# Performance work log

Measured on AMD Instinct MI355X. Metric: run time of the kernel, lower is better.

## Reference

```python
import jax, jax.numpy as jnp
import numpy as np

HIDDEN = 256
N_HEADS = 8
HEAD_DIM = HIDDEN // N_HEADS
SCALE = HEAD_DIM ** -0.5
LN_EPS = 1e-5


def entmax15(z):
    """Entmax-1.5 along the last axis (Peters et al. 2019 exact algorithm)."""
    z = z / 2.0
    z = z - jnp.max(z, axis=-1, keepdims=True)
    zs = jnp.flip(jnp.sort(z, axis=-1), axis=-1)          # descending
    K = z.shape[-1]
    k = jnp.arange(1, K + 1, dtype=z.dtype)
    mean = jnp.cumsum(zs, axis=-1) / k
    mean_sq = jnp.cumsum(zs * zs, axis=-1) / k
    ss = k * (mean_sq - mean * mean)
    delta = (1.0 - ss) / k
    tau = mean - jnp.sqrt(jnp.maximum(delta, 1e-12))
    support = (tau <= zs).astype(jnp.int32)
    k_star = jnp.sum(support, axis=-1, keepdims=True)      # support size >=1
    tau_star = jnp.take_along_axis(tau, k_star - 1, axis=-1)
    p = jnp.square(jnp.maximum(z - tau_star, 0.0))
    return p


def _attend(q, kv, W_q, W_k, W_v, log_temp):
    B, K, H = kv.shape
    qh = (q @ W_q.T).reshape(B, N_HEADS, HEAD_DIM)                 # (B,n,d)
    kh = (kv @ W_k.T).reshape(B, K, N_HEADS, HEAD_DIM)             # (B,K,n,d)
    vh = (kv @ W_v.T).reshape(B, K, N_HEADS, HEAD_DIM)
    scores = jnp.einsum('bnd,bknd->bnk', qh, kh) * (SCALE * jnp.exp(log_temp))
    attn = entmax15(scores)                                        # (B,n,K) sparse
    ctx = jnp.einsum('bnk,bknd->bnd', attn, vh).reshape(B, H)
    return ctx


def layernorm(x, gamma, beta):
    mu = jnp.mean(x, axis=-1, keepdims=True)
    var = jnp.mean(jnp.square(x - mu), axis=-1, keepdims=True)
    return (x - mu) * jax.lax.rsqrt(var + LN_EPS) * gamma + beta


def setup_inputs() -> dict:
    key = jax.random.key(0)
    ks = jax.random.split(key, 12)
    B, K, H = 32, 8192, HIDDEN
    s = 0.02
    return {
        'z_gene': jax.random.normal(ks[0], (B, H), jnp.float32),
        'z_cpg_seq': jax.random.normal(ks[1], (B, K, H), jnp.float32),
        'z_mirna_seq': jax.random.normal(ks[2], (B, K, H), jnp.float32),
        'W_q': jax.random.normal(ks[3], (H, H), jnp.float32) * s,
        'W_k_cpg': jax.random.normal(ks[4], (H, H), jnp.float32) * s,
        'W_v_cpg': jax.random.normal(ks[5], (H, H), jnp.float32) * s,
        'W_k_mirna': jax.random.normal(ks[6], (H, H), jnp.float32) * s,
        'W_v_mirna': jax.random.normal(ks[7], (H, H), jnp.float32) * s,
        'W_out': jax.random.normal(ks[8], (H, 2 * H), jnp.float32) * s,
        'b_out': jnp.zeros((H,), jnp.float32),
        'ln_gamma': jnp.ones((H,), jnp.float32),
        'ln_beta': jnp.zeros((H,), jnp.float32),
        'modality_logits': jnp.zeros((2,), jnp.float32),
        'log_temp': jnp.zeros((), jnp.float32),
    }


def reference(z_gene, z_cpg_seq, z_mirna_seq, W_q, W_k_cpg, W_v_cpg,
              W_k_mirna, W_v_mirna, W_out, b_out, ln_gamma, ln_beta,
              modality_logits, log_temp):
    ctx_cpg = _attend(z_gene, z_cpg_seq, W_q, W_k_cpg, W_v_cpg, log_temp)
    ctx_mirna = _attend(z_gene, z_mirna_seq, W_q, W_k_mirna, W_v_mirna, log_temp)
    w = jax.nn.softmax(modality_logits)
    combined = jnp.concatenate([w[0] * ctx_cpg, w[1] * ctx_mirna], axis=-1)
    fused = layernorm(combined @ W_out.T + b_out + z_gene, ln_gamma, ln_beta)
    return fused
```

## Files before the change

kernel.cpp:

```cpp
#include <hip/hip_runtime.h>
#include <cstdint>
#include <cstddef>

#define HIDDEN 256
#define NHEADS 8
#define HDIM 32
#define KLEN 8192
#define BATCH 32
#define NCHUNK 16
#define CHUNK (KLEN / NCHUNK)
#define LN_EPS 1e-5f

#define OFF_QT   ((size_t)0)
#define SZ_QT    ((size_t)2*BATCH*NHEADS*HIDDEN)
#define OFF_SC   (OFF_QT + SZ_QT)
#define SZ_SC    ((size_t)2*BATCH*KLEN*NHEADS)
#define OFF_TAU  (OFF_SC + SZ_SC)
#define SZ_TAU   ((size_t)2*BATCH*NHEADS)
#define OFF_UP   (OFF_TAU + SZ_TAU)
#define SZ_UP    ((size_t)2*BATCH*NCHUNK*NHEADS*HIDDEN)
#define OFF_COMB (OFF_UP + SZ_UP)
#define SZ_COMB  ((size_t)BATCH*2*HIDDEN)

__global__ void k_prep(const float* __restrict__ zg, const float* __restrict__ Wq,
                       const float* __restrict__ Wk0, const float* __restrict__ Wk1,
                       const float* __restrict__ log_temp, float* __restrict__ qt) {
    int b = blockIdx.x, t = threadIdx.x;
    __shared__ float z[HIDDEN];
    __shared__ float qh[HIDDEN];
    z[t] = zg[(size_t)b*HIDDEN + t];
    __syncthreads();
    const float4* wr4 = (const float4*)(Wq + (size_t)t*HIDDEN);
    const float4* z4 = (const float4*)z;
    float acc = 0.f;
    #pragma unroll 8
    for (int i = 0; i < HIDDEN/4; ++i) {
        float4 w = wr4[i], zz = z4[i];
        acc += w.x*zz.x + w.y*zz.y + w.z*zz.z + w.w*zz.w;
    }
    qh[t] = acc;
    __syncthreads();
    float alpha = 0.5f * rsqrtf((float)HDIM) * __expf(log_temp[0]);
    for (int m = 0; m < 2; ++m) {
        const float* Wk = m ? Wk1 : Wk0;
        for (int n = 0; n < NHEADS; ++n) {
            float a = 0.f;
            #pragma unroll 8
            for (int d = 0; d < HDIM; ++d) {
                a += qh[n*HDIM + d] * Wk[(size_t)(n*HDIM + d)*HIDDEN + t];
            }
            qt[(((size_t)m*BATCH + b)*NHEADS + n)*HIDDEN + t] = a * alpha;
        }
    }
}

__global__ void __launch_bounds__(256) k_scores(const float* __restrict__ kv0,
                                                const float* __restrict__ kv1,
                                                const float* __restrict__ qt,
                                                float* __restrict__ sc) {
    int bid = blockIdx.x;
    int chunk = bid % NCHUNK;
    int m = (bid / NCHUNK) & 1;
    int b = bid / (2*NCHUNK);
    int t = threadIdx.x;
    int wave = t >> 6;
    int g    = (t >> 3) & 7;
    int seg  = t & 7;
    __shared__ float lq[NHEADS*260];
    const float* qtg = qt + ((size_t)m*BATCH + b)*NHEADS*HIDDEN;
    #pragma unroll
    for (int i = 0; i < 8; ++i) {
        int j = t + i*256;
        lq[(j >> 8)*260 + (j & 255)] = qtg[j];
    }
    __syncthreads();
    const float* kv = (m ? kv1 : kv0) + (size_t)b*KLEN*HIDDEN;
    const float4* kv4 = (const float4*)kv;
    float* out = sc + ((size_t)m*BATCH + b)*KLEN*NHEADS;
    int b0 = seg & 1, b1 = (seg >> 1) & 1, b2 = (seg >> 2) & 1;

    int rowbase = chunk*CHUNK + wave*128;
    for (int pass = 0; pass < 8; ++pass) {
        size_t r0 = (size_t)rowbase + pass*16 + g*2;
        size_t r1 = r0 + 1;
        float4 kva[8], kvb[8];
        #pragma unroll
        for (int i = 0; i < 8; ++i) kva[i] = kv4[r0*64 + i*8 + seg];
        #pragma unroll
        for (int i = 0; i < 8; ++i) kvb[i] = kv4[r1*64 + i*8 + seg];
        float acc0[8], acc1[8];
        #pragma unroll
        for (int n = 0; n < 8; ++n) { acc0[n] = 0.f; acc1[n] = 0.f; }
        #pragma unroll
        for (int n = 0; n < 8; ++n) {
            const float4* qn4 = (const float4*)(lq + n*260);
            #pragma unroll
            for (int i = 0; i < 8; ++i) {
                float4 q = qn4[i*8 + seg];
                acc0[n] += kva[i].x*q.x + kva[i].y*q.y + kva[i].z*q.z + kva[i].w*q.w;
                acc1[n] += kvb[i].x*q.x + kvb[i].y*q.y + kvb[i].z*q.z + kvb[i].w*q.w;
            }
        }
        float w0[4], w1[4];
        #pragma unroll
        for (int j = 0; j < 4; ++j) {
            float k0 = b0 ? acc0[2*j+1] : acc0[2*j];
            float s0 = b0 ? acc0[2*j]   : acc0[2*j+1];
            w0[j] = k0 + __shfl_xor(s0, 1);
            float k1 = b0 ? acc1[2*j+1] : acc1[2*j];
            float s1 = b0 ? acc1[2*j]   : acc1[2*j+1];
            w1[j] = k1 + __shfl_xor(s1, 1);
        }
        float x0[2], x1[2];
        #pragma unroll
        for (int j = 0; j < 2; ++j) {
            float k0 = b1 ? w0[2*j+1] : w0[2*j];
            float s0 = b1 ? w0[2*j]   : w0[2*j+1];
            x0[j] = k0 + __shfl_xor(s0, 2);
            float k1 = b1 ? w1[2*j+1] : w1[2*j];
            float s1 = b1 ? w1[2*j]   : w1[2*j+1];
            x1[j] = k1 + __shfl_xor(s1, 2);
        }
        float ka = b2 ? x0[1] : x0[0];
        float sa = b2 ? x0[0] : x0[1];
        float y0 = ka + __shfl_xor(sa, 4);
        float kb = b2 ? x1[1] : x1[0];
        float sb = b2 ? x1[0] : x1[1];
        float y1 = kb + __shfl_xor(sb, 4);
        out[r0*8 + seg] = y0;
        out[r1*8 + seg] = y1;
    }
}

__global__ void __launch_bounds__(256) k_entmax(const float* __restrict__ sc,
                                                float* __restrict__ tau) {
    int bid = blockIdx.x;
    int n = bid & 7, b = (bid >> 3) & 31, m = bid >> 8;
    int t = threadIdx.x;
    __shared__ float zs[KLEN];
    __shared__ float red[4];
    const float* src = sc + ((size_t)m*BATCH + b)*KLEN*NHEADS + n;
    float mx = -1e30f;
    #pragma unroll
    for (int i = 0; i < KLEN/256; ++i) {
        float v = src[(size_t)(t + i*256)*NHEADS];
        zs[t + i*256] = v;
        mx = fmaxf(mx, v);
    }
    for (int off = 32; off; off >>= 1) mx = fmaxf(mx, __shfl_xor(mx, off));
    if ((t & 63) == 0) red[t >> 6] = mx;
    __syncthreads();
    mx = fmaxf(fmaxf(red[0], red[1]), fmaxf(red[2], red[3]));
    __syncthreads();
    const float4* z4 = (const float4*)zs;
    float lo = mx - 1.0f, hi = mx;
    for (int it = 0; it < 30; ++it) {
        float tm = 0.5f*(lo + hi);
        float s = 0.f;
        #pragma unroll
        for (int i = 0; i < 8; ++i) {
            float4 zz = z4[t + i*256];
            float d;
            d = fmaxf(zz.x - tm, 0.f); s = fmaf(d, d, s);
            d = fmaxf(zz.y - tm, 0.f); s = fmaf(d, d, s);
            d = fmaxf(zz.z - tm, 0.f); s = fmaf(d, d, s);
            d = fmaxf(zz.w - tm, 0.f); s = fmaf(d, d, s);
        }
        for (int off = 32; off; off >>= 1) s += __shfl_xor(s, off);
        if ((t & 63) == 0) red[t >> 6] = s;
        __syncthreads();
        s = red[0] + red[1] + red[2] + red[3];
        __syncthreads();
        if (s >= 1.0f) lo = tm; else hi = tm;
    }
    if (t == 0) tau[bid] = 0.5f*(lo + hi);
}

__global__ void __launch_bounds__(256) k_ctxsum(const float* __restrict__ kv0,
                                                const float* __restrict__ kv1,
                                                const float* __restrict__ sc,
                                                const float* __restrict__ tau,
                                                float* __restrict__ upart) {
    int bid = blockIdx.x;
    int chunk = bid % NCHUNK;
    int m = (bid / NCHUNK) & 1;
    int b = bid / (2*NCHUNK);
    int t = threadIdx.x;
    int wave = t >> 6, lane = t & 63;
    const float* kv = (m ? kv1 : kv0) + (size_t)b*KLEN*HIDDEN;
    const float4* kv4 = (const float4*)kv;
    const float* zrow = sc + ((size_t)m*BATCH + b)*KLEN*NHEADS;
    const float4* zrow4 = (const float4*)zrow;
    float tv[8];
    #pragma unroll
    for (int n = 0; n < 8; ++n) tv[n] = tau[((size_t)m*BATCH + b)*NHEADS + n];
    float acc[8][4];
    #pragma unroll
    for (int n = 0; n < 8; ++n)
        #pragma unroll
        for (int c = 0; c < 4; ++c) acc[n][c] = 0.f;

    #pragma unroll 2
    for (int kk = wave; kk < CHUNK; kk += 4) {
        size_t k = (size_t)chunk*CHUNK + kk;
        float4 kvv = kv4[k*64 + lane];
        float4 za = zrow4[k*2], zb = zrow4[k*2 + 1];
        float p[8], d;
        d = fmaxf(za.x - tv[0], 0.f); p[0] = d*d;
        d = fmaxf(za.y - tv[1], 0.f); p[1] = d*d;
        d = fmaxf(za.z - tv[2], 0.f); p[2] = d*d;
        d = fmaxf(za.w - tv[3], 0.f); p[3] = d*d;
        d = fmaxf(zb.x - tv[4], 0.f); p[4] = d*d;
        d = fmaxf(zb.y - tv[5], 0.f); p[5] = d*d;
        d = fmaxf(zb.z - tv[6], 0.f); p[6] = d*d;
        d = fmaxf(zb.w - tv[7], 0.f); p[7] = d*d;
        #pragma unroll
        for (int n = 0; n < 8; ++n) {
            acc[n][0] = fmaf(p[n], kvv.x, acc[n][0]);
            acc[n][1] = fmaf(p[n], kvv.y, acc[n][1]);
            acc[n][2] = fmaf(p[n], kvv.z, acc[n][2]);
            acc[n][3] = fmaf(p[n], kvv.w, acc[n][3]);
        }
    }
    __shared__ float redls[4*NHEADS*HIDDEN];
    float4* red4 = (float4*)redls;
    #pragma unroll
    for (int n = 0; n < 8; ++n) {
        float4 v; v.x = acc[n][0]; v.y = acc[n][1]; v.z = acc[n][2]; v.w = acc[n][3];
        red4[((size_t)wave*8 + n)*64 + lane] = v;
    }
    __syncthreads();
    float* up = upart + (((size_t)m*BATCH + b)*NCHUNK + chunk)*NHEADS*HIDDEN;
    int n = t >> 5, hq = (t & 31)*2;
    #pragma unroll
    for (int j = 0; j < 2; ++j) {
        float4 s = red4[((size_t)0*8 + n)*64 + hq + j];
        #pragma unroll
        for (int w = 1; w < 4; ++w) {
            float4 v = red4[((size_t)w*8 + n)*64 + hq + j];
            s.x += v.x; s.y += v.y; s.z += v.z; s.w += v.w;
        }
        ((float4*)(up + (size_t)n*HIDDEN))[hq + j] = s;
    }
}

__global__ void k_ctx(const float* __restrict__ upart, const float* __restrict__ Wv0,
                      const float* __restrict__ Wv1, const float* __restrict__ mlogits,
                      float* __restrict__ comb) {
    int b = blockIdx.x, t = threadIdx.x;
    __shared__ float ul[NHEADS*260];
    float l0 = mlogits[0], l1 = mlogits[1];
    float mxl = fmaxf(l0, l1);
    float e0 = __expf(l0 - mxl), e1 = __expf(l1 - mxl);
    float w0 = e0/(e0 + e1), w1 = e1/(e0 + e1);
    for (int m = 0; m < 2; ++m) {
        const float* Wv = m ? Wv1 : Wv0;
        float wm = m ? w1 : w0;
        __syncthreads();
        for (int n = 0; n < NHEADS; ++n) {
            float s = 0.f;
            const float* up = upart + ((size_t)m*BATCH + b)*NCHUNK*NHEADS*HIDDEN
                              + (size_t)n*HIDDEN + t;
            #pragma unroll
            for (int c = 0; c < NCHUNK; ++c) s += up[(size_t)c*NHEADS*HIDDEN];
            ul[n*260 + t] = s;
        }
        __syncthreads();
        int n = t >> 5;
        const float4* wr4 = (const float4*)(Wv + (size_t)t*HIDDEN);
        const float4* uu4 = (const float4*)(ul + n*260);
        float acc = 0.f;
        #pragma unroll 8
        for (int i = 0; i < HIDDEN/4; ++i) {
            float4 w = wr4[i], uu = uu4[i];
            acc += w.x*uu.x + w.y*uu.y + w.z*uu.z + w.w*uu.w;
        }
        comb[(size_t)b*(2*HIDDEN) + (size_t)m*HIDDEN + t] = acc * wm;
    }
}

__global__ void k_out(const float* __restrict__ comb, const float* __restrict__ Wout,
                      const float* __restrict__ bout, const float* __restrict__ zg,
                      const float* __restrict__ gamma, const float* __restrict__ beta,
                      float* __restrict__ out) {
    int b = blockIdx.x, t = threadIdx.x;
    __shared__ float cl[2*HIDDEN];
    __shared__ float red[4];
    cl[t] = comb[(size_t)b*512 + t];
    cl[t + 256] = comb[(size_t)b*512 + 256 + t];
    __syncthreads();
    float acc = bout[t] + zg[(size_t)b*HIDDEN + t];
    const float4* wr4 = (const float4*)(Wout + (size_t)t*512);
    const float4* cl4 = (const float4*)cl;
    #pragma unroll 8
    for (int i = 0; i < 512/4; ++i) {
        float4 w = wr4[i], c = cl4[i];
        acc += w.x*c.x + w.y*c.y + w.z*c.z + w.w*c.w;
    }
    float s = acc;
    for (int off = 32; off; off >>= 1) s += __shfl_xor(s, off);
    if ((t & 63) == 0) red[t >> 6] = s;
    __syncthreads();
    float mu = (red[0] + red[1] + red[2] + red[3]) * (1.0f/HIDDEN);
    __syncthreads();
    float dv = acc - mu;
    float vs = dv*dv;
    for (int off = 32; off; off >>= 1) vs += __shfl_xor(vs, off);
    if ((t & 63) == 0) red[t >> 6] = vs;
    __syncthreads();
    float var = (red[0] + red[1] + red[2] + red[3]) * (1.0f/HIDDEN);
    out[(size_t)b*HIDDEN + t] = dv * rsqrtf(var + LN_EPS) * gamma[t] + beta[t];
}

extern "C" void kernel_launch(void* const* d_in, const int* in_sizes, int n_in,
                              void* d_out, int out_size, void* d_ws, size_t ws_size,
                              hipStream_t stream) {
    const float* zg    = (const float*)d_in[0];
    const float* cpg   = (const float*)d_in[1];
    const float* mir   = (const float*)d_in[2];
    const float* Wq    = (const float*)d_in[3];
    const float* Wk0   = (const float*)d_in[4];
    const float* Wv0   = (const float*)d_in[5];
    const float* Wk1   = (const float*)d_in[6];
    const float* Wv1   = (const float*)d_in[7];
    const float* Wout  = (const float*)d_in[8];
    const float* bout  = (const float*)d_in[9];
    const float* gam   = (const float*)d_in[10];
    const float* bet   = (const float*)d_in[11];
    const float* mlog  = (const float*)d_in[12];
    const float* ltemp = (const float*)d_in[13];

    float* ws   = (float*)d_ws;
    float* qt   = ws + OFF_QT;
    float* sc   = ws + OFF_SC;
    float* tau  = ws + OFF_TAU;
    float* up   = ws + OFF_UP;
    float* comb = ws + OFF_COMB;
    float* out  = (float*)d_out;

    hipLaunchKernelGGL(k_prep,   dim3(BATCH),            dim3(256), 0, stream,
                       zg, Wq, Wk0, Wk1, ltemp, qt);
    hipLaunchKernelGGL(k_scores, dim3(BATCH*2*NCHUNK),   dim3(256), 0, stream,
                       cpg, mir, qt, sc);
    hipLaunchKernelGGL(k_entmax, dim3(2*BATCH*NHEADS),   dim3(256), 0, stream,
                       sc, tau);
    hipLaunchKernelGGL(k_ctxsum, dim3(BATCH*2*NCHUNK),   dim3(256), 0, stream,
                       cpg, mir, sc, tau, up);
    hipLaunchKernelGGL(k_ctx,    dim3(BATCH),            dim3(256), 0, stream,
                       up, Wv0, Wv1, mlog, comb);
    hipLaunchKernelGGL(k_out,    dim3(BATCH),            dim3(256), 0, stream,
                       comb, Wout, bout, zg, gam, bet, out);
}
```

Before: 322.0 us.

## Retile score and context kernels, write entmax probabilities in place, trim bisection

The scores kernel now uses 32 chunks per sequence and each thread handles four rows per pass, so each query element read from shared memory is reused across four rows; it also gets occupancy launch bounds. The entmax kernel runs 26 bisection steps instead of 30 and writes the final probabilities over the scores buffer, so the context-sum kernel no longer recomputes the thresholded squares and the tau buffer is removed. The context-sum kernel processes four rows per iteration, walks blocks in reverse order (likely to hit KV data still in cache from the scores pass), and declares occupancy bounds. Fewer bisection steps give a slightly less precise threshold.

```diff
diff --git a/kernel.cpp b/kernel.cpp
--- a/kernel.cpp
+++ b/kernel.cpp
@@ -9,15 +9,15 @@
 #define BATCH 32
 #define NCHUNK 16
 #define CHUNK (KLEN / NCHUNK)
+#define NCHUNK_S 32
+#define CROWS (KLEN / NCHUNK_S)
 #define LN_EPS 1e-5f
 
 #define OFF_QT   ((size_t)0)
 #define SZ_QT    ((size_t)2*BATCH*NHEADS*HIDDEN)
 #define OFF_SC   (OFF_QT + SZ_QT)
 #define SZ_SC    ((size_t)2*BATCH*KLEN*NHEADS)
-#define OFF_TAU  (OFF_SC + SZ_SC)
-#define SZ_TAU   ((size_t)2*BATCH*NHEADS)
-#define OFF_UP   (OFF_TAU + SZ_TAU)
+#define OFF_UP   (OFF_SC + SZ_SC)
 #define SZ_UP    ((size_t)2*BATCH*NCHUNK*NHEADS*HIDDEN)
 #define OFF_COMB (OFF_UP + SZ_UP)
 #define SZ_COMB  ((size_t)BATCH*2*HIDDEN)
@@ -54,14 +54,14 @@
     }
 }
 
-__global__ void __launch_bounds__(256) k_scores(const float* __restrict__ kv0,
-                                                const float* __restrict__ kv1,
-                                                const float* __restrict__ qt,
-                                                float* __restrict__ sc) {
+__global__ void __launch_bounds__(256, 4) k_scores(const float* __restrict__ kv0,
+                                                   const float* __restrict__ kv1,
+                                                   const float* __restrict__ qt,
+                                                   float* __restrict__ sc) {
     int bid = blockIdx.x;
-    int chunk = bid % NCHUNK;
-    int m = (bid / NCHUNK) & 1;
-    int b = bid / (2*NCHUNK);
+    int chunk = bid % NCHUNK_S;
+    int m = (bid / NCHUNK_S) & 1;
+    int b = bid / (2*NCHUNK_S);
     int t = threadIdx.x;
     int wave = t >> 6;
     int g    = (t >> 3) & 7;
@@ -79,67 +79,61 @@
     float* out = sc + ((size_t)m*BATCH + b)*KLEN*NHEADS;
     int b0 = seg & 1, b1 = (seg >> 1) & 1, b2 = (seg >> 2) & 1;
 
-    int rowbase = chunk*CHUNK + wave*128;
-    for (int pass = 0; pass < 8; ++pass) {
-        size_t r0 = (size_t)rowbase + pass*16 + g*2;
-        size_t r1 = r0 + 1;
-        float4 kva[8], kvb[8];
-        #pragma unroll
-        for (int i = 0; i < 8; ++i) kva[i] = kv4[r0*64 + i*8 + seg];
-        #pragma unroll
-        for (int i = 0; i < 8; ++i) kvb[i] = kv4[r1*64 + i*8 + seg];
-        float acc0[8], acc1[8];
-        #pragma unroll
-        for (int n = 0; n < 8; ++n) { acc0[n] = 0.f; acc1[n] = 0.f; }
-        #pragma unroll
-        for (int n = 0; n < 8; ++n) {
-            const float4* qn4 = (const float4*)(lq + n*260);
-            #pragma unroll
-            for (int i = 0; i < 8; ++i) {
-                float4 q = qn4[i*8 + seg];
-                acc0[n] += kva[i].x*q.x + kva[i].y*q.y + kva[i].z*q.z + kva[i].w*q.w;
-                acc1[n] += kvb[i].x*q.x + kvb[i].y*q.y + kvb[i].z*q.z + kvb[i].w*q.w;
+    #pragma unroll
+    for (int pass = 0; pass < 2; ++pass) {
+        size_t r = (size_t)chunk*CROWS + wave*64 + pass*32 + g*4;
+        float acc[4][8];
+        #pragma unroll
+        for (int j = 0; j < 4; ++j)
+            #pragma unroll
+            for (int n = 0; n < 8; ++n) acc[j][n] = 0.f;
+        #pragma unroll 2
+        for (int i = 0; i < 8; ++i) {
+            int c = i*8 + seg;
+            float4 k0 = kv4[(r+0)*64 + c];
+            float4 k1 = kv4[(r+1)*64 + c];
+            float4 k2 = kv4[(r+2)*64 + c];
+            float4 k3 = kv4[(r+3)*64 + c];
+            #pragma unroll
+            for (int n = 0; n < 8; ++n) {
+                float4 q = ((const float4*)(lq + n*260))[c];
+                acc[0][n] += k0.x*q.x + k0.y*q.y + k0.z*q.z + k0.w*q.w;
+                acc[1][n] += k1.x*q.x + k1.y*q.y + k1.z*q.z + k1.w*q.w;
+                acc[2][n] += k2.x*q.x + k2.y*q.y + k2.z*q.z + k2.w*q.w;
+                acc[3][n] += k3.x*q.x + k3.y*q.y + k3.z*q.z + k3.w*q.w;
             }
         }
-        float w0[4], w1[4];
         #pragma unroll
         for (int j = 0; j < 4; ++j) {
-            float k0 = b0 ? acc0[2*j+1] : acc0[2*j];
-            float s0 = b0 ? acc0[2*j]   : acc0[2*j+1];
-            w0[j] = k0 + __shfl_xor(s0, 1);
-            float k1 = b0 ? acc1[2*j+1] : acc1[2*j];
-            float s1 = b0 ? acc1[2*j]   : acc1[2*j+1];
-            w1[j] = k1 + __shfl_xor(s1, 1);
-        }
-        float x0[2], x1[2];
-        #pragma unroll
-        for (int j = 0; j < 2; ++j) {
-            float k0 = b1 ? w0[2*j+1] : w0[2*j];
-            float s0 = b1 ? w0[2*j]   : w0[2*j+1];
-            x0[j] = k0 + __shfl_xor(s0, 2);
-            float k1 = b1 ? w1[2*j+1] : w1[2*j];
-            float s1 = b1 ? w1[2*j]   : w1[2*j+1];
-            x1[j] = k1 + __shfl_xor(s1, 2);
-        }
-        float ka = b2 ? x0[1] : x0[0];
-        float sa = b2 ? x0[0] : x0[1];
-        float y0 = ka + __shfl_xor(sa, 4);
-        float kb = b2 ? x1[1] : x1[0];
-        float sb = b2 ? x1[0] : x1[1];
-        float y1 = kb + __shfl_xor(sb, 4);
-        out[r0*8 + seg] = y0;
-        out[r1*8 + seg] = y1;
-    }
-}
-
-__global__ void __launch_bounds__(256) k_entmax(const float* __restrict__ sc,
-                                                float* __restrict__ tau) {
+            float w[4];
+            #pragma unroll
+            for (int u = 0; u < 4; ++u) {
+                float kkeep = b0 ? acc[j][2*u+1] : acc[j][2*u];
+                float ksend = b0 ? acc[j][2*u]   : acc[j][2*u+1];
+                w[u] = kkeep + __shfl_xor(ksend, 1);
+            }
+            float x[2];
+            #pragma unroll
+            for (int u = 0; u < 2; ++u) {
+                float kkeep = b1 ? w[2*u+1] : w[2*u];
+                float ksend = b1 ? w[2*u]   : w[2*u+1];
+                x[u] = kkeep + __shfl_xor(ksend, 2);
+            }
+            float kkeep = b2 ? x[1] : x[0];
+            float ksend = b2 ? x[0] : x[1];
+            float y = kkeep + __shfl_xor(ksend, 4);
+            out[(r+j)*8 + seg] = y;
+        }
+    }
+}
+
+__global__ void __launch_bounds__(256) k_entmax(float* __restrict__ sc) {
     int bid = blockIdx.x;
     int n = bid & 7, b = (bid >> 3) & 31, m = bid >> 8;
     int t = threadIdx.x;
     __shared__ float zs[KLEN];
     __shared__ float red[4];
-    const float* src = sc + ((size_t)m*BATCH + b)*KLEN*NHEADS + n;
+    float* src = sc + ((size_t)m*BATCH + b)*KLEN*NHEADS + n;
     float mx = -1e30f;
     #pragma unroll
     for (int i = 0; i < KLEN/256; ++i) {
@@ -154,7 +148,7 @@
     __syncthreads();
     const float4* z4 = (const float4*)zs;
     float lo = mx - 1.0f, hi = mx;
-    for (int it = 0; it < 30; ++it) {
+    for (int it = 0; it < 26; ++it) {
         float tm = 0.5f*(lo + hi);
         float s = 0.f;
         #pragma unroll
@@ -173,15 +167,19 @@
         __syncthreads();
         if (s >= 1.0f) lo = tm; else hi = tm;
     }
-    if (t == 0) tau[bid] = 0.5f*(lo + hi);
-}
-
-__global__ void __launch_bounds__(256) k_ctxsum(const float* __restrict__ kv0,
-                                                const float* __restrict__ kv1,
-                                                const float* __restrict__ sc,
-                                                const float* __restrict__ tau,
-                                                float* __restrict__ upart) {
-    int bid = blockIdx.x;
+    float tfin = 0.5f*(lo + hi);
+    #pragma unroll
+    for (int i = 0; i < KLEN/256; ++i) {
+        float d = fmaxf(zs[t + i*256] - tfin, 0.f);
+        src[(size_t)(t + i*256)*NHEADS] = d*d;
+    }
+}
+
+__global__ void __launch_bounds__(256, 4) k_ctxsum(const float* __restrict__ kv0,
+                                                   const float* __restrict__ kv1,
+                                                   const float* __restrict__ sc,
+                                                   float* __restrict__ upart) {
+    int bid = (int)gridDim.x - 1 - (int)blockIdx.x;
     int chunk = bid % NCHUNK;
     int m = (bid / NCHUNK) & 1;
     int b = bid / (2*NCHUNK);
@@ -189,45 +187,52 @@
     int wave = t >> 6, lane = t & 63;
     const float* kv = (m ? kv1 : kv0) + (size_t)b*KLEN*HIDDEN;
     const float4* kv4 = (const float4*)kv;
-    const float* zrow = sc + ((size_t)m*BATCH + b)*KLEN*NHEADS;
-    const float4* zrow4 = (const float4*)zrow;
-    float tv[8];
-    #pragma unroll
-    for (int n = 0; n < 8; ++n) tv[n] = tau[((size_t)m*BATCH + b)*NHEADS + n];
+    const float4* prow4 = (const float4*)(sc + ((size_t)m*BATCH + b)*KLEN*NHEADS);
     float acc[8][4];
     #pragma unroll
-    for (int n = 0; n < 8; ++n)
-        #pragma unroll
-        for (int c = 0; c < 4; ++c) acc[n][c] = 0.f;
-
-    #pragma unroll 2
-    for (int kk = wave; kk < CHUNK; kk += 4) {
-        size_t k = (size_t)chunk*CHUNK + kk;
-        float4 kvv = kv4[k*64 + lane];
-        float4 za = zrow4[k*2], zb = zrow4[k*2 + 1];
-        float p[8], d;
-        d = fmaxf(za.x - tv[0], 0.f); p[0] = d*d;
-        d = fmaxf(za.y - tv[1], 0.f); p[1] = d*d;
-        d = fmaxf(za.z - tv[2], 0.f); p[2] = d*d;
-        d = fmaxf(za.w - tv[3], 0.f); p[3] = d*d;
-        d = fmaxf(zb.x - tv[4], 0.f); p[4] = d*d;
-        d = fmaxf(zb.y - tv[5], 0.f); p[5] = d*d;
-        d = fmaxf(zb.z - tv[6], 0.f); p[6] = d*d;
-        d = fmaxf(zb.w - tv[7], 0.f); p[7] = d*d;
-        #pragma unroll
-        for (int n = 0; n < 8; ++n) {
-            acc[n][0] = fmaf(p[n], kvv.x, acc[n][0]);
-            acc[n][1] = fmaf(p[n], kvv.y, acc[n][1]);
-            acc[n][2] = fmaf(p[n], kvv.z, acc[n][2]);
-            acc[n][3] = fmaf(p[n], kvv.w, acc[n][3]);
-        }
+    for (int nn = 0; nn < 8; ++nn)
+        #pragma unroll
+        for (int c = 0; c < 4; ++c) acc[nn][c] = 0.f;
+
+    for (int kb = wave*4; kb < CHUNK; kb += 16) {
+        size_t k = (size_t)chunk*CHUNK + kb;
+        float4 kva = kv4[(k+0)*64 + lane];
+        float4 kvb = kv4[(k+1)*64 + lane];
+        float4 kvc = kv4[(k+2)*64 + lane];
+        float4 kvd = kv4[(k+3)*64 + lane];
+        float4 pa0 = prow4[(k+0)*2], pa1 = prow4[(k+0)*2 + 1];
+        float4 pb0 = prow4[(k+1)*2], pb1 = prow4[(k+1)*2 + 1];
+        float4 pc0 = prow4[(k+2)*2], pc1 = prow4[(k+2)*2 + 1];
+        float4 pd0 = prow4[(k+3)*2], pd1 = prow4[(k+3)*2 + 1];
+        #define ACC4(P0, P1, KV) \
+            acc[0][0] = fmaf(P0.x, KV.x, acc[0][0]); acc[0][1] = fmaf(P0.x, KV.y, acc[0][1]); \
+            acc[0][2] = fmaf(P0.x, KV.z, acc[0][2]); acc[0][3] = fmaf(P0.x, KV.w, acc[0][3]); \
+            acc[1][0] = fmaf(P0.y, KV.x, acc[1][0]); acc[1][1] = fmaf(P0.y, KV.y, acc[1][1]); \
+            acc[1][2] = fmaf(P0.y, KV.z, acc[1][2]); acc[1][3] = fmaf(P0.y, KV.w, acc[1][3]); \
+            acc[2][0] = fmaf(P0.z, KV.x, acc[2][0]); acc[2][1] = fmaf(P0.z, KV.y, acc[2][1]); \
+            acc[2][2] = fmaf(P0.z, KV.z, acc[2][2]); acc[2][3] = fmaf(P0.z, KV.w, acc[2][3]); \
+            acc[3][0] = fmaf(P0.w, KV.x, acc[3][0]); acc[3][1] = fmaf(P0.w, KV.y, acc[3][1]); \
+            acc[3][2] = fmaf(P0.w, KV.z, acc[3][2]); acc[3][3] = fmaf(P0.w, KV.w, acc[3][3]); \
+            acc[4][0] = fmaf(P1.x, KV.x, acc[4][0]); acc[4][1] = fmaf(P1.x, KV.y, acc[4][1]); \
+            acc[4][2] = fmaf(P1.x, KV.z, acc[4][2]); acc[4][3] = fmaf(P1.x, KV.w, acc[4][3]); \
+            acc[5][0] = fmaf(P1.y, KV.x, acc[5][0]); acc[5][1] = fmaf(P1.y, KV.y, acc[5][1]); \
+            acc[5][2] = fmaf(P1.y, KV.z, acc[5][2]); acc[5][3] = fmaf(P1.y, KV.w, acc[5][3]); \
+            acc[6][0] = fmaf(P1.z, KV.x, acc[6][0]); acc[6][1] = fmaf(P1.z, KV.y, acc[6][1]); \
+            acc[6][2] = fmaf(P1.z, KV.z, acc[6][2]); acc[6][3] = fmaf(P1.z, KV.w, acc[6][3]); \
+            acc[7][0] = fmaf(P1.w, KV.x, acc[7][0]); acc[7][1] = fmaf(P1.w, KV.y, acc[7][1]); \
+            acc[7][2] = fmaf(P1.w, KV.z, acc[7][2]); acc[7][3] = fmaf(P1.w, KV.w, acc[7][3]);
+        ACC4(pa0, pa1, kva)
+        ACC4(pb0, pb1, kvb)
+        ACC4(pc0, pc1, kvc)
+        ACC4(pd0, pd1, kvd)
+        #undef ACC4
     }
     __shared__ float redls[4*NHEADS*HIDDEN];
     float4* red4 = (float4*)redls;
     #pragma unroll
-    for (int n = 0; n < 8; ++n) {
-        float4 v; v.x = acc[n][0]; v.y = acc[n][1]; v.z = acc[n][2]; v.w = acc[n][3];
-        red4[((size_t)wave*8 + n)*64 + lane] = v;
+    for (int nn = 0; nn < 8; ++nn) {
+        float4 v; v.x = acc[nn][0]; v.y = acc[nn][1]; v.z = acc[nn][2]; v.w = acc[nn][3];
+        red4[((size_t)wave*8 + nn)*64 + lane] = v;
     }
     __syncthreads();
     float* up = upart + (((size_t)m*BATCH + b)*NCHUNK + chunk)*NHEADS*HIDDEN;
@@ -333,21 +338,20 @@
     float* ws   = (float*)d_ws;
     float* qt   = ws + OFF_QT;
     float* sc   = ws + OFF_SC;
-    float* tau  = ws + OFF_TAU;
     float* up   = ws + OFF_UP;
     float* comb = ws + OFF_COMB;
     float* out  = (float*)d_out;
 
-    hipLaunchKernelGGL(k_prep,   dim3(BATCH),            dim3(256), 0, stream,
+    hipLaunchKernelGGL(k_prep,   dim3(BATCH),             dim3(256), 0, stream,
                        zg, Wq, Wk0, Wk1, ltemp, qt);
-    hipLaunchKernelGGL(k_scores, dim3(BATCH*2*NCHUNK),   dim3(256), 0, stream,
+    hipLaunchKernelGGL(k_scores, dim3(BATCH*2*NCHUNK_S),  dim3(256), 0, stream,
                        cpg, mir, qt, sc);
-    hipLaunchKernelGGL(k_entmax, dim3(2*BATCH*NHEADS),   dim3(256), 0, stream,
-                       sc, tau);
-    hipLaunchKernelGGL(k_ctxsum, dim3(BATCH*2*NCHUNK),   dim3(256), 0, stream,
-                       cpg, mir, sc, tau, up);
-    hipLaunchKernelGGL(k_ctx,    dim3(BATCH),            dim3(256), 0, stream,
+    hipLaunchKernelGGL(k_entmax, dim3(2*BATCH*NHEADS),    dim3(256), 0, stream,
+                       sc);
+    hipLaunchKernelGGL(k_ctxsum, dim3(BATCH*2*NCHUNK),    dim3(256), 0, stream,
+                       cpg, mir, sc, up);
+    hipLaunchKernelGGL(k_ctx,    dim3(BATCH),             dim3(256), 0, stream,
                        up, Wv0, Wv1, mlog, comb);
-    hipLaunchKernelGGL(k_out,    dim3(BATCH),            dim3(256), 0, stream,
+    hipLaunchKernelGGL(k_out,    dim3(BATCH),             dim3(256), 0, stream,
                        comb, Wout, bout, zg, gam, bet, out);
 }
```

After: 338.4 us. +5.1%, slower.
